# Optimization experiments

Measured on AMD Instinct MI355X. Metric: run time of the kernel, lower is better.

## Reference

```python
import jax, jax.numpy as jnp
import numpy as np

FEAT = 1024   # feat_dim
EMB = 64      # emb_dim
GROUP = 16    # group == fc_dim
DG = FEAT // GROUP  # 64, per-group query/key dim and conv out channels per group
R = 1024      # num_rois
N = 1024      # nongt_dim


def setup_inputs() -> dict:
    key = jax.random.key(0)
    ks = jax.random.split(key, 8)
    inp = {
        "position_embedding": jax.random.normal(ks[0], (R, N, EMB), dtype=jnp.float32),
        "roi_feat": jax.random.normal(ks[1], (R, FEAT), dtype=jnp.float32),
        # fc_q / fc_k: Linear(feat_dim, feat_dim)
        "Wq": jax.random.normal(ks[2], (FEAT, FEAT), dtype=jnp.float32) * 0.02,
        "bq": jnp.zeros((FEAT,), dtype=jnp.float32),
        "Wk": jax.random.normal(ks[3], (FEAT, FEAT), dtype=jnp.float32) * 0.02,
        "bk": jnp.zeros((FEAT,), dtype=jnp.float32),
        # fc_pos_feat: Linear(emb_dim, fc_dim=group)
        "Wp": jax.random.normal(ks[4], (GROUP, EMB), dtype=jnp.float32) * 0.1,
        "bp": jnp.zeros((GROUP,), dtype=jnp.float32),
        # conv_cat: Conv2d(group*feat_dim, feat_dim, k=1, groups=group)
        # per group g: in FEAT channels -> out DG channels. Shape [GROUP, DG, FEAT].
        "Wc": jax.random.normal(ks[5], (GROUP, DG, FEAT), dtype=jnp.float32) * 0.02,
        "bc": jnp.zeros((FEAT,), dtype=jnp.float32),
        "nongt_dim": N,
    }
    return inp


def reference(position_embedding, roi_feat, Wq, bq, Wk, bk, Wp, bp, Wc, bc, nongt_dim):
    scale = 1.0 / np.sqrt(float(DG))
    # fc_pos_feat + relu -> aff_weight [R, GROUP, N]
    pos_feat = jax.nn.relu(jnp.einsum("rne,ge->rng", position_embedding, Wp) + bp)
    aff_weight = jnp.transpose(pos_feat, (0, 2, 1))  # [R, GROUP, N]
    nongt = roi_feat[:nongt_dim]                     # [N, FEAT]
    q = (roi_feat @ Wq.T + bq).reshape(-1, GROUP, DG)   # [R, GROUP, DG]
    k = (nongt @ Wk.T + bk).reshape(-1, GROUP, DG)      # [N, GROUP, DG]
    # per-group QK^T with log position bias
    aff = jnp.einsum("rgd,ngd->rgn", q, k) * scale      # [R, GROUP, N]
    weighted = jnp.log(jnp.clip(aff_weight, 1e-6, None)) + aff
    att = jax.nn.softmax(weighted, axis=2)              # [R, GROUP, N]
    # attention * V -> [R, GROUP, FEAT]
    out_t = jnp.einsum("rgn,nf->rgf", att, nongt)
    # grouped 1x1 conv combine: group g maps FEAT -> DG output channels
    out = jnp.einsum("rgf,gof->rgo", out_t, Wc).reshape(-1, FEAT) + bc
    return out
```

## Files before the change

kernel.cpp:

```cpp
#include <hip/hip_runtime.h>

#define R_DIM 1024
#define N_DIM 1024
#define FEAT  1024
#define EMB   64
#define GROUP 16
#define DG    64

typedef _Float16 half8  __attribute__((ext_vector_type(8)));
typedef _Float16 half4v __attribute__((ext_vector_type(4)));
typedef float    f32x4  __attribute__((ext_vector_type(4)));

__global__ __launch_bounds__(256) void qk_gemm(
    const float* __restrict__ roi, const float* __restrict__ Wq,
    const float* __restrict__ bq,  const float* __restrict__ Wk,
    const float* __restrict__ bk,  _Float16* __restrict__ qh,
    _Float16* __restrict__ kh)
{
  __shared__ float aT[16][68];
  __shared__ float bqT[16][68];
  __shared__ float bkT[16][68];
  const int t  = threadIdx.x;
  const int r0 = blockIdx.x * 64, c0 = blockIdx.y * 64;
  const int lr = t >> 2, lk = (t & 3) << 2;
  const int ty = t >> 4, tx = t & 15;
  const float* ap  = roi + (r0 + lr) * FEAT + lk;
  const float* bqp = Wq  + (c0 + lr) * FEAT + lk;
  const float* bkp = Wk  + (c0 + lr) * FEAT + lk;
  float4 av  = *(const float4*)ap;
  float4 bqv = *(const float4*)bqp;
  float4 bkv = *(const float4*)bkp;
  float accq[4][4] = {}, acck[4][4] = {};
  for (int k0 = 0; k0 < FEAT; k0 += 16) {
    aT[lk+0][lr]=av.x;   aT[lk+1][lr]=av.y;   aT[lk+2][lr]=av.z;   aT[lk+3][lr]=av.w;
    bqT[lk+0][lr]=bqv.x; bqT[lk+1][lr]=bqv.y; bqT[lk+2][lr]=bqv.z; bqT[lk+3][lr]=bqv.w;
    bkT[lk+0][lr]=bkv.x; bkT[lk+1][lr]=bkv.y; bkT[lk+2][lr]=bkv.z; bkT[lk+3][lr]=bkv.w;
    __syncthreads();
    const bool more = (k0 + 16) < FEAT;
    float4 av_n, bqv_n, bkv_n;
    if (more) {
      av_n  = *(const float4*)(ap  + k0 + 16);
      bqv_n = *(const float4*)(bqp + k0 + 16);
      bkv_n = *(const float4*)(bkp + k0 + 16);
    }
#pragma unroll
    for (int kk = 0; kk < 16; ++kk) {
      const float4 a4 = *(const float4*)&aT[kk][ty << 2];
      const float4 q4 = *(const float4*)&bqT[kk][tx << 2];
      const float4 k4 = *(const float4*)&bkT[kk][tx << 2];
      const float ar[4] = {a4.x, a4.y, a4.z, a4.w};
      const float qr[4] = {q4.x, q4.y, q4.z, q4.w};
      const float kr[4] = {k4.x, k4.y, k4.z, k4.w};
#pragma unroll
      for (int i = 0; i < 4; ++i)
#pragma unroll
        for (int j = 0; j < 4; ++j) {
          accq[i][j] += ar[i] * qr[j];
          acck[i][j] += ar[i] * kr[j];
        }
    }
    __syncthreads();
    if (more) { av = av_n; bqv = bqv_n; bkv = bkv_n; }
  }
  const float4 bq4 = *(const float4*)(bq + c0 + (tx << 2));
  const float4 bk4 = *(const float4*)(bk + c0 + (tx << 2));
  const float bqr[4] = {bq4.x, bq4.y, bq4.z, bq4.w};
  const float bkr[4] = {bk4.x, bk4.y, bk4.z, bk4.w};
#pragma unroll
  for (int i = 0; i < 4; ++i) {
    half4v oq, ok;
#pragma unroll
    for (int j = 0; j < 4; ++j) {
      oq[j] = (_Float16)(accq[i][j] + bqr[j]);
      ok[j] = (_Float16)(acck[i][j] + bkr[j]);
    }
    const int row = r0 + (ty << 2) + i;
    *(half4v*)(qh + (size_t)row * FEAT + c0 + (tx << 2)) = oq;
    *(half4v*)(kh + (size_t)row * FEAT + c0 + (tx << 2)) = ok;
  }
}

__global__ __launch_bounds__(128) void pos_log(
    const float* __restrict__ pe, const float* __restrict__ Wp,
    const float* __restrict__ bp, _Float16* __restrict__ logw)
{
  __shared__ float tile[128 * 68];
  const int t    = threadIdx.x;
  const int base = blockIdx.x << 7;
  const int r    = base >> 10;
  const int n0   = base & 1023;
  const float* src = pe + ((size_t)base << 6);
#pragma unroll
  for (int i = 0; i < 16; ++i) {
    const int flat = (i << 7) + t;
    const int rl = flat >> 4, e4 = flat & 15;
    const float4 v = *(const float4*)(src + ((size_t)flat << 2));
    *(float4*)&tile[rl * 68 + (e4 << 2)] = v;
  }
  __syncthreads();
  float acc[16];
#pragma unroll
  for (int g = 0; g < 16; ++g) acc[g] = bp[g];
#pragma unroll
  for (int e4 = 0; e4 < 16; ++e4) {
    const float4 x = *(const float4*)&tile[t * 68 + (e4 << 2)];
#pragma unroll
    for (int g = 0; g < 16; ++g) {
      const float4 w = *(const float4*)(Wp + (g << 6) + (e4 << 2));
      acc[g] += x.x*w.x + x.y*w.y + x.z*w.z + x.w*w.w;
    }
  }
  const int n = n0 + t;
#pragma unroll
  for (int g = 0; g < 16; ++g) {
    const float v = fmaxf(acc[g], 1e-6f);
    logw[((size_t)((r << 4) + g) << 10) + n] = (_Float16)__logf(v);
  }
}

__global__ __launch_bounds__(256) void kc_gemm(
    const float* __restrict__ roi, const float* __restrict__ Wc,
    _Float16* __restrict__ kct)
{
  __shared__ float aT[16][68];
  __shared__ float bT[16][68];
  const int t  = threadIdx.x;
  const int n0 = blockIdx.x * 64;
  const int g  = blockIdx.y;
  const int lr = t >> 2, lk = (t & 3) << 2;
  const int ty = t >> 4, tx = t & 15;
  const float* ap  = Wc  + (size_t)(g * DG + lr) * FEAT + lk;
  const float* bp_ = roi + (size_t)(n0 + lr) * FEAT + lk;
  float4 av = *(const float4*)ap;
  float4 bv = *(const float4*)bp_;
  float acc[4][4] = {};
  for (int k0 = 0; k0 < FEAT; k0 += 16) {
    aT[lk+0][lr]=av.x; aT[lk+1][lr]=av.y; aT[lk+2][lr]=av.z; aT[lk+3][lr]=av.w;
    bT[lk+0][lr]=bv.x; bT[lk+1][lr]=bv.y; bT[lk+2][lr]=bv.z; bT[lk+3][lr]=bv.w;
    __syncthreads();
    const bool more = (k0 + 16) < FEAT;
    float4 av_n, bv_n;
    if (more) {
      av_n = *(const float4*)(ap  + k0 + 16);
      bv_n = *(const float4*)(bp_ + k0 + 16);
    }
#pragma unroll
    for (int kk = 0; kk < 16; ++kk) {
      const float4 a4 = *(const float4*)&aT[kk][ty << 2];
      const float4 b4 = *(const float4*)&bT[kk][tx << 2];
      const float ar[4] = {a4.x, a4.y, a4.z, a4.w};
      const float br[4] = {b4.x, b4.y, b4.z, b4.w};
#pragma unroll
      for (int i = 0; i < 4; ++i)
#pragma unroll
        for (int j = 0; j < 4; ++j) acc[i][j] += ar[i] * br[j];
    }
    __syncthreads();
    if (more) { av = av_n; bv = bv_n; }
  }
#pragma unroll
  for (int i = 0; i < 4; ++i) {
    half4v o4;
#pragma unroll
    for (int j = 0; j < 4; ++j) o4[j] = (_Float16)acc[i][j];
    *(half4v*)(kct + (size_t)((g << 6) + (ty << 2) + i) * N_DIM + n0 + (tx << 2)) = o4;
  }
}

#define PLD 1032
__global__ __launch_bounds__(256) void attn_mfma(
    const _Float16* __restrict__ qh, const _Float16* __restrict__ kh,
    const _Float16* __restrict__ logw, const _Float16* __restrict__ kct,
    const float* __restrict__ bc, float* __restrict__ outp)
{
  __shared__ __align__(16) _Float16 P[16][PLD];
  __shared__ float Ored[4][16][68];
  __shared__ float redm[4][16];
  __shared__ float redl[4][16];

  const int t   = threadIdx.x;
  const int w   = t >> 6;
  const int l   = t & 63;
  const int q16 = l & 15;
  const int q4  = l >> 4;
  const int g   = blockIdx.y;
  const int r0  = blockIdx.x << 4;
  const int nbase = w << 8;

  const half8* qp = (const half8*)(qh + (size_t)(r0 + q16) * FEAT + (g << 6) + (q4 << 3));
  const half8 a0 = qp[0];
  const half8 a1 = qp[4];

  f32x4 S[16];
#pragma unroll
  for (int i = 0; i < 16; ++i) S[i] = (f32x4){0.f, 0.f, 0.f, 0.f};
#pragma unroll
  for (int t16 = 0; t16 < 16; ++t16) {
    const int n0 = nbase + (t16 << 4);
    const half8* kp = (const half8*)(kh + (size_t)(n0 + q16) * FEAT + (g << 6) + (q4 << 3));
    S[t16] = __builtin_amdgcn_mfma_f32_16x16x32_f16(a0, kp[0], S[t16], 0, 0, 0);
    S[t16] = __builtin_amdgcn_mfma_f32_16x16x32_f16(a1, kp[4], S[t16], 0, 0, 0);
  }

#pragma unroll
  for (int t16 = 0; t16 < 16; ++t16) {
    const int n = nbase + (t16 << 4) + q16;
#pragma unroll
    for (int j = 0; j < 4; ++j) {
      const int r = r0 + (q4 << 2) + j;
      const float lw = (float)logw[(size_t)(((r << 4) + g) << 10) + n];
      S[t16][j] = S[t16][j] * 0.125f + lw;
    }
  }

  float m[4] = {-1e30f, -1e30f, -1e30f, -1e30f};
#pragma unroll
  for (int t16 = 0; t16 < 16; ++t16)
#pragma unroll
    for (int j = 0; j < 4; ++j) m[j] = fmaxf(m[j], S[t16][j]);
#pragma unroll
  for (int off = 8; off; off >>= 1)
#pragma unroll
    for (int j = 0; j < 4; ++j) m[j] = fmaxf(m[j], __shfl_xor(m[j], off));
  if (q16 == 0) {
#pragma unroll
    for (int j = 0; j < 4; ++j) redm[w][(q4 << 2) + j] = m[j];
  }
  __syncthreads();
#pragma unroll
  for (int j = 0; j < 4; ++j) {
    const int r = (q4 << 2) + j;
    m[j] = fmaxf(fmaxf(redm[0][r], redm[1][r]), fmaxf(redm[2][r], redm[3][r]));
  }

  float ls[4] = {0.f, 0.f, 0.f, 0.f};
#pragma unroll
  for (int t16 = 0; t16 < 16; ++t16) {
    const int n = nbase + (t16 << 4) + q16;
#pragma unroll
    for (int j = 0; j < 4; ++j) {
      const float p = __expf(S[t16][j] - m[j]);
      ls[j] += p;
      P[(q4 << 2) + j][n] = (_Float16)p;
    }
  }
#pragma unroll
  for (int off = 8; off; off >>= 1)
#pragma unroll
    for (int j = 0; j < 4; ++j) ls[j] += __shfl_xor(ls[j], off);
  if (q16 == 0) {
#pragma unroll
    for (int j = 0; j < 4; ++j) redl[w][(q4 << 2) + j] = ls[j];
  }
  __syncthreads();

  f32x4 O[4];
#pragma unroll
  for (int ot = 0; ot < 4; ++ot) O[ot] = (f32x4){0.f, 0.f, 0.f, 0.f};
#pragma unroll
  for (int ks = 0; ks < 8; ++ks) {
    const int nk = nbase + (ks << 5) + (q4 << 3);
    const half8 pa = *(const half8*)&P[q16][nk];
#pragma unroll
    for (int ot = 0; ot < 4; ++ot) {
      const half8 bfr = *(const half8*)(kct + (size_t)((g << 6) + (ot << 4) + q16) * N_DIM + nk);
      O[ot] = __builtin_amdgcn_mfma_f32_16x16x32_f16(pa, bfr, O[ot], 0, 0, 0);
    }
  }
#pragma unroll
  for (int ot = 0; ot < 4; ++ot)
#pragma unroll
    for (int j = 0; j < 4; ++j)
      Ored[w][(q4 << 2) + j][(ot << 4) + q16] = O[ot][j];
  __syncthreads();

  const int r  = t >> 4;
  const int o0 = (t & 15) << 2;
  const float lsum = redl[0][r] + redl[1][r] + redl[2][r] + redl[3][r];
  const float inv  = 1.0f / lsum;
  float o[4];
#pragma unroll
  for (int c = 0; c < 4; ++c)
    o[c] = Ored[0][r][o0 + c] + Ored[1][r][o0 + c] + Ored[2][r][o0 + c] + Ored[3][r][o0 + c];
  const float4 bcv = *(const float4*)(bc + (g << 6) + o0);
  float4 res;
  res.x = o[0] * inv + bcv.x;
  res.y = o[1] * inv + bcv.y;
  res.z = o[2] * inv + bcv.z;
  res.w = o[3] * inv + bcv.w;
  *(float4*)(outp + (size_t)(r0 + r) * FEAT + (g << 6) + o0) = res;
}

extern "C" void kernel_launch(void* const* d_in, const int* in_sizes, int n_in,
                              void* d_out, int out_size, void* d_ws, size_t ws_size,
                              hipStream_t stream)
{
  const float* pe  = (const float*)d_in[0];
  const float* roi = (const float*)d_in[1];
  const float* Wq  = (const float*)d_in[2];
  const float* bq  = (const float*)d_in[3];
  const float* Wk  = (const float*)d_in[4];
  const float* bk  = (const float*)d_in[5];
  const float* Wp  = (const float*)d_in[6];
  const float* bp  = (const float*)d_in[7];
  const float* Wc  = (const float*)d_in[8];
  const float* bc  = (const float*)d_in[9];
  float* outp = (float*)d_out;

  char* ws = (char*)d_ws;
  _Float16* qh   = (_Float16*)(ws);
  _Float16* kh   = (_Float16*)(ws + ((size_t)2 << 20));
  _Float16* kct  = (_Float16*)(ws + ((size_t)4 << 20));
  _Float16* logw = (_Float16*)(ws + ((size_t)6 << 20));

  qk_gemm<<<dim3(16, 16), 256, 0, stream>>>(roi, Wq, bq, Wk, bk, qh, kh);
  pos_log<<<8192, 128, 0, stream>>>(pe, Wp, bp, logw);
  kc_gemm<<<dim3(16, 16), 256, 0, stream>>>(roi, Wc, kct);
  attn_mfma<<<dim3(64, 16), 256, 0, stream>>>(qh, kh, logw, kct, bc, outp);
}
```

Measured before the change: 229.1 us.

## Merge producer kernels into one launch with MFMA GEMMs and restructured pos_log

Replaces the three producer kernels (Q/K projection, position-log, Wc·roi GEMM) with a single kernel whose block index picks the role. The GEMM roles now use fp16 MFMA 16x16x32 instructions, converting fp32 operands straight from global memory with no LDS staging. The position-log role keeps the transposed Wp in LDS and splits the embedding dimension across 4 lanes, reducing with shuffles. This cuts launch count and moves the projections onto matrix cores, at the cost of fp16 rounding of the GEMM inputs and uncoalesced strided loads and scalar fp16 stores.

```diff
diff --git a/kernel.cpp b/kernel.cpp
--- a/kernel.cpp
+++ b/kernel.cpp
@@ -11,159 +11,120 @@
 typedef _Float16 half4v __attribute__((ext_vector_type(4)));
 typedef float    f32x4  __attribute__((ext_vector_type(4)));
 
-__global__ __launch_bounds__(256) void qk_gemm(
+__device__ __forceinline__ half8 cvt8(const float* p) {
+  const float4 a = *(const float4*)p;
+  const float4 b = *(const float4*)(p + 4);
+  half8 h;
+  h[0] = (_Float16)a.x; h[1] = (_Float16)a.y; h[2] = (_Float16)a.z; h[3] = (_Float16)a.w;
+  h[4] = (_Float16)b.x; h[5] = (_Float16)b.y; h[6] = (_Float16)b.z; h[7] = (_Float16)b.w;
+  return h;
+}
+
+__global__ __launch_bounds__(256) void producers(
     const float* __restrict__ roi, const float* __restrict__ Wq,
     const float* __restrict__ bq,  const float* __restrict__ Wk,
-    const float* __restrict__ bk,  _Float16* __restrict__ qh,
-    _Float16* __restrict__ kh)
+    const float* __restrict__ bk,  const float* __restrict__ Wc,
+    const float* __restrict__ pe,  const float* __restrict__ Wp,
+    const float* __restrict__ bp,
+    _Float16* __restrict__ qh, _Float16* __restrict__ kh,
+    _Float16* __restrict__ kct, _Float16* __restrict__ logw)
 {
-  __shared__ float aT[16][68];
-  __shared__ float bqT[16][68];
-  __shared__ float bkT[16][68];
+  __shared__ float lds_w[4 * 264];
+  const int bx = blockIdx.x;
   const int t  = threadIdx.x;
-  const int r0 = blockIdx.x * 64, c0 = blockIdx.y * 64;
-  const int lr = t >> 2, lk = (t & 3) << 2;
-  const int ty = t >> 4, tx = t & 15;
-  const float* ap  = roi + (r0 + lr) * FEAT + lk;
-  const float* bqp = Wq  + (c0 + lr) * FEAT + lk;
-  const float* bkp = Wk  + (c0 + lr) * FEAT + lk;
-  float4 av  = *(const float4*)ap;
-  float4 bqv = *(const float4*)bqp;
-  float4 bkv = *(const float4*)bkp;
-  float accq[4][4] = {}, acck[4][4] = {};
-  for (int k0 = 0; k0 < FEAT; k0 += 16) {
-    aT[lk+0][lr]=av.x;   aT[lk+1][lr]=av.y;   aT[lk+2][lr]=av.z;   aT[lk+3][lr]=av.w;
-    bqT[lk+0][lr]=bqv.x; bqT[lk+1][lr]=bqv.y; bqT[lk+2][lr]=bqv.z; bqT[lk+3][lr]=bqv.w;
-    bkT[lk+0][lr]=bkv.x; bkT[lk+1][lr]=bkv.y; bkT[lk+2][lr]=bkv.z; bkT[lk+3][lr]=bkv.w;
+
+  if (bx < 768) {
+    const float* A; const float* B; const float* bias;
+    _Float16* outb; int r0, c0;
+    if (bx < 256) {
+      A = roi; B = Wq; bias = bq; outb = qh;
+      r0 = (bx >> 4) << 6; c0 = (bx & 15) << 6;
+    } else if (bx < 512) {
+      const int i = bx - 256;
+      A = roi; B = Wk; bias = bk; outb = kh;
+      r0 = (i >> 4) << 6; c0 = (i & 15) << 6;
+    } else {
+      const int i = bx - 512, g = i >> 4;
+      A = Wc + ((size_t)g << 16); B = roi; bias = nullptr;
+      outb = kct + ((size_t)g << 16);
+      r0 = 0; c0 = (i & 15) << 6;
+    }
+    const int wv = t >> 6, l = t & 63, q16 = l & 15, q4 = l >> 4;
+    const float* ap  = A + (size_t)(r0 + (wv << 4) + q16) * FEAT + (q4 << 3);
+    const float* bp0 = B + (size_t)(c0 + q16) * FEAT + (q4 << 3);
+
+    f32x4 acc[4];
+#pragma unroll
+    for (int ct = 0; ct < 4; ++ct) acc[ct] = (f32x4){0.f, 0.f, 0.f, 0.f};
+
+    for (int kk = 0; kk < FEAT; kk += 32) {
+      const half8 a = cvt8(ap + kk);
+#pragma unroll
+      for (int ct = 0; ct < 4; ++ct) {
+        const half8 b = cvt8(bp0 + (size_t)(ct << 4) * FEAT + kk);
+        acc[ct] = __builtin_amdgcn_mfma_f32_16x16x32_f16(a, b, acc[ct], 0, 0, 0);
+      }
+    }
+#pragma unroll
+    for (int ct = 0; ct < 4; ++ct) {
+      const int col = c0 + (ct << 4) + q16;
+      const float bv = bias ? bias[col] : 0.f;
+#pragma unroll
+      for (int j = 0; j < 4; ++j) {
+        const int row = r0 + (wv << 4) + (q4 << 2) + j;
+        outb[(size_t)row * FEAT + col] = (_Float16)(acc[ct][j] + bv);
+      }
+    }
+  } else {
+    {
+      const float4 v = ((const float4*)Wp)[t];
+      const int l4s = (t & 15) >> 2, ib = (t & 3) << 2, g = t >> 4;
+#pragma unroll
+      for (int c = 0; c < 4; ++c)
+        lds_w[l4s * 264 + (ib + c) * 16 + g] = ((const float*)&v)[c];
+    }
     __syncthreads();
-    const bool more = (k0 + 16) < FEAT;
-    float4 av_n, bqv_n, bkv_n;
-    if (more) {
-      av_n  = *(const float4*)(ap  + k0 + 16);
-      bqv_n = *(const float4*)(bqp + k0 + 16);
-      bkv_n = *(const float4*)(bkp + k0 + 16);
-    }
-#pragma unroll
-    for (int kk = 0; kk < 16; ++kk) {
-      const float4 a4 = *(const float4*)&aT[kk][ty << 2];
-      const float4 q4 = *(const float4*)&bqT[kk][tx << 2];
-      const float4 k4 = *(const float4*)&bkT[kk][tx << 2];
-      const float ar[4] = {a4.x, a4.y, a4.z, a4.w};
-      const float qr[4] = {q4.x, q4.y, q4.z, q4.w};
-      const float kr[4] = {k4.x, k4.y, k4.z, k4.w};
-#pragma unroll
-      for (int i = 0; i < 4; ++i)
-#pragma unroll
-        for (int j = 0; j < 4; ++j) {
-          accq[i][j] += ar[i] * qr[j];
-          acck[i][j] += ar[i] * kr[j];
+    const int w = t >> 6, l = t & 63, r16 = l >> 2, l4 = l & 3;
+    const float4 bpv = *(const float4*)(bp + (l4 << 2));
+    const int pb = bx - 768;
+#pragma unroll 1
+    for (int it = 0; it < 8; ++it) {
+      const int rowb = ((pb << 5) + (w << 3) + it) << 4;
+      const int row  = rowb + r16;
+      const float* src = pe + ((size_t)row << 6) + (l4 << 4);
+      float x[16];
+      *(float4*)&x[0]  = *(const float4*)(src);
+      *(float4*)&x[4]  = *(const float4*)(src + 4);
+      *(float4*)&x[8]  = *(const float4*)(src + 8);
+      *(float4*)&x[12] = *(const float4*)(src + 12);
+      float acc[16];
+#pragma unroll
+      for (int g = 0; g < 16; ++g) acc[g] = 0.f;
+#pragma unroll
+      for (int i = 0; i < 16; ++i) {
+#pragma unroll
+        for (int g4 = 0; g4 < 4; ++g4) {
+          const float4 w4 = *(const float4*)&lds_w[l4 * 264 + i * 16 + (g4 << 2)];
+          acc[(g4 << 2) + 0] += x[i] * w4.x;
+          acc[(g4 << 2) + 1] += x[i] * w4.y;
+          acc[(g4 << 2) + 2] += x[i] * w4.z;
+          acc[(g4 << 2) + 3] += x[i] * w4.w;
         }
-    }
-    __syncthreads();
-    if (more) { av = av_n; bqv = bqv_n; bkv = bkv_n; }
-  }
-  const float4 bq4 = *(const float4*)(bq + c0 + (tx << 2));
-  const float4 bk4 = *(const float4*)(bk + c0 + (tx << 2));
-  const float bqr[4] = {bq4.x, bq4.y, bq4.z, bq4.w};
-  const float bkr[4] = {bk4.x, bk4.y, bk4.z, bk4.w};
-#pragma unroll
-  for (int i = 0; i < 4; ++i) {
-    half4v oq, ok;
-#pragma unroll
-    for (int j = 0; j < 4; ++j) {
-      oq[j] = (_Float16)(accq[i][j] + bqr[j]);
-      ok[j] = (_Float16)(acck[i][j] + bkr[j]);
-    }
-    const int row = r0 + (ty << 2) + i;
-    *(half4v*)(qh + (size_t)row * FEAT + c0 + (tx << 2)) = oq;
-    *(half4v*)(kh + (size_t)row * FEAT + c0 + (tx << 2)) = ok;
-  }
-}
-
-__global__ __launch_bounds__(128) void pos_log(
-    const float* __restrict__ pe, const float* __restrict__ Wp,
-    const float* __restrict__ bp, _Float16* __restrict__ logw)
-{
-  __shared__ float tile[128 * 68];
-  const int t    = threadIdx.x;
-  const int base = blockIdx.x << 7;
-  const int r    = base >> 10;
-  const int n0   = base & 1023;
-  const float* src = pe + ((size_t)base << 6);
-#pragma unroll
-  for (int i = 0; i < 16; ++i) {
-    const int flat = (i << 7) + t;
-    const int rl = flat >> 4, e4 = flat & 15;
-    const float4 v = *(const float4*)(src + ((size_t)flat << 2));
-    *(float4*)&tile[rl * 68 + (e4 << 2)] = v;
-  }
-  __syncthreads();
-  float acc[16];
-#pragma unroll
-  for (int g = 0; g < 16; ++g) acc[g] = bp[g];
-#pragma unroll
-  for (int e4 = 0; e4 < 16; ++e4) {
-    const float4 x = *(const float4*)&tile[t * 68 + (e4 << 2)];
-#pragma unroll
-    for (int g = 0; g < 16; ++g) {
-      const float4 w = *(const float4*)(Wp + (g << 6) + (e4 << 2));
-      acc[g] += x.x*w.x + x.y*w.y + x.z*w.z + x.w*w.w;
-    }
-  }
-  const int n = n0 + t;
-#pragma unroll
-  for (int g = 0; g < 16; ++g) {
-    const float v = fmaxf(acc[g], 1e-6f);
-    logw[((size_t)((r << 4) + g) << 10) + n] = (_Float16)__logf(v);
-  }
-}
-
-__global__ __launch_bounds__(256) void kc_gemm(
-    const float* __restrict__ roi, const float* __restrict__ Wc,
-    _Float16* __restrict__ kct)
-{
-  __shared__ float aT[16][68];
-  __shared__ float bT[16][68];
-  const int t  = threadIdx.x;
-  const int n0 = blockIdx.x * 64;
-  const int g  = blockIdx.y;
-  const int lr = t >> 2, lk = (t & 3) << 2;
-  const int ty = t >> 4, tx = t & 15;
-  const float* ap  = Wc  + (size_t)(g * DG + lr) * FEAT + lk;
-  const float* bp_ = roi + (size_t)(n0 + lr) * FEAT + lk;
-  float4 av = *(const float4*)ap;
-  float4 bv = *(const float4*)bp_;
-  float acc[4][4] = {};
-  for (int k0 = 0; k0 < FEAT; k0 += 16) {
-    aT[lk+0][lr]=av.x; aT[lk+1][lr]=av.y; aT[lk+2][lr]=av.z; aT[lk+3][lr]=av.w;
-    bT[lk+0][lr]=bv.x; bT[lk+1][lr]=bv.y; bT[lk+2][lr]=bv.z; bT[lk+3][lr]=bv.w;
-    __syncthreads();
-    const bool more = (k0 + 16) < FEAT;
-    float4 av_n, bv_n;
-    if (more) {
-      av_n = *(const float4*)(ap  + k0 + 16);
-      bv_n = *(const float4*)(bp_ + k0 + 16);
-    }
-#pragma unroll
-    for (int kk = 0; kk < 16; ++kk) {
-      const float4 a4 = *(const float4*)&aT[kk][ty << 2];
-      const float4 b4 = *(const float4*)&bT[kk][tx << 2];
-      const float ar[4] = {a4.x, a4.y, a4.z, a4.w};
-      const float br[4] = {b4.x, b4.y, b4.z, b4.w};
-#pragma unroll
-      for (int i = 0; i < 4; ++i)
-#pragma unroll
-        for (int j = 0; j < 4; ++j) acc[i][j] += ar[i] * br[j];
-    }
-    __syncthreads();
-    if (more) { av = av_n; bv = bv_n; }
-  }
-#pragma unroll
-  for (int i = 0; i < 4; ++i) {
-    half4v o4;
-#pragma unroll
-    for (int j = 0; j < 4; ++j) o4[j] = (_Float16)acc[i][j];
-    *(half4v*)(kct + (size_t)((g << 6) + (ty << 2) + i) * N_DIM + n0 + (tx << 2)) = o4;
+      }
+#pragma unroll
+      for (int g = 0; g < 16; ++g) {
+        acc[g] += __shfl_xor(acc[g], 1);
+        acc[g] += __shfl_xor(acc[g], 2);
+      }
+      const int r = row >> 10, n = row & 1023;
+      _Float16* dst = logw + ((size_t)(r << 4) << 10) + n;
+#pragma unroll
+      for (int c = 0; c < 4; ++c) {
+        const int g = (l4 << 2) + c;
+        const float v = fmaxf(acc[g] + ((const float*)&bpv)[c], 1e-6f);
+        dst[(size_t)g << 10] = (_Float16)__logf(v);
+      }
+    }
   }
 }
 
@@ -313,8 +274,7 @@
   _Float16* kct  = (_Float16*)(ws + ((size_t)4 << 20));
   _Float16* logw = (_Float16*)(ws + ((size_t)6 << 20));
 
-  qk_gemm<<<dim3(16, 16), 256, 0, stream>>>(roi, Wq, bq, Wk, bk, qh, kh);
-  pos_log<<<8192, 128, 0, stream>>>(pe, Wp, bp, logw);
-  kc_gemm<<<dim3(16, 16), 256, 0, stream>>>(roi, Wc, kct);
+  producers<<<2816, 256, 0, stream>>>(roi, Wq, bq, Wk, bk, Wc, pe, Wp, bp,
+                                      qh, kh, kct, logw);
   attn_mfma<<<dim3(64, 16), 256, 0, stream>>>(qh, kh, logw, kct, bc, outp);
 }
```

Measured after the change: 292.7 us. 27.7% more time.

## Compute position-embedding projection with fp16 MFMA and coalesced transposed stores

Applied to the files above, without the earlier changes.

Replaces the scalar FP32 pos_log kernel with pos_mfma. It converts each 128x64 position-embedding tile to fp16 in an XOR-swizzled LDS buffer and computes the 16-group projection with 16x16x32 f16 MFMA instructions. The log outputs are staged in LDS and written as coalesced half8 rows, replacing the earlier scattered 2-byte stores. The aim is to make this 256MB-read stage bandwidth-bound rather than ALU-bound. The cost is reduced precision in the projection inputs, which are now rounded to fp16.

```diff
diff --git a/kernel.cpp b/kernel.cpp
--- a/kernel.cpp
+++ b/kernel.cpp
@@ -10,6 +10,15 @@
 typedef _Float16 half8  __attribute__((ext_vector_type(8)));
 typedef _Float16 half4v __attribute__((ext_vector_type(4)));
 typedef float    f32x4  __attribute__((ext_vector_type(4)));
+
+__device__ __forceinline__ half8 cvt8(const float* p) {
+  const float4 a = *(const float4*)p;
+  const float4 b = *(const float4*)(p + 4);
+  half8 h;
+  h[0] = (_Float16)a.x; h[1] = (_Float16)a.y; h[2] = (_Float16)a.z; h[3] = (_Float16)a.w;
+  h[4] = (_Float16)b.x; h[5] = (_Float16)b.y; h[6] = (_Float16)b.z; h[7] = (_Float16)b.w;
+  return h;
+}
 
 __global__ __launch_bounds__(256) void qk_gemm(
     const float* __restrict__ roi, const float* __restrict__ Wq,
@@ -80,42 +89,61 @@
   }
 }
 
-__global__ __launch_bounds__(128) void pos_log(
+__global__ __launch_bounds__(256) void pos_mfma(
     const float* __restrict__ pe, const float* __restrict__ Wp,
     const float* __restrict__ bp, _Float16* __restrict__ logw)
 {
-  __shared__ float tile[128 * 68];
-  const int t    = threadIdx.x;
-  const int base = blockIdx.x << 7;
-  const int r    = base >> 10;
-  const int n0   = base & 1023;
-  const float* src = pe + ((size_t)base << 6);
-#pragma unroll
-  for (int i = 0; i < 16; ++i) {
-    const int flat = (i << 7) + t;
-    const int rl = flat >> 4, e4 = flat & 15;
-    const float4 v = *(const float4*)(src + ((size_t)flat << 2));
-    *(float4*)&tile[rl * 68 + (e4 << 2)] = v;
-  }
-  __syncthreads();
-  float acc[16];
-#pragma unroll
-  for (int g = 0; g < 16; ++g) acc[g] = bp[g];
-#pragma unroll
-  for (int e4 = 0; e4 < 16; ++e4) {
-    const float4 x = *(const float4*)&tile[t * 68 + (e4 << 2)];
-#pragma unroll
-    for (int g = 0; g < 16; ++g) {
-      const float4 w = *(const float4*)(Wp + (g << 6) + (e4 << 2));
-      acc[g] += x.x*w.x + x.y*w.y + x.z*w.z + x.w*w.w;
-    }
-  }
-  const int n = n0 + t;
-#pragma unroll
-  for (int g = 0; g < 16; ++g) {
-    const float v = fmaxf(acc[g], 1e-6f);
-    logw[((size_t)((r << 4) + g) << 10) + n] = (_Float16)__logf(v);
-  }
+  __shared__ __align__(16) _Float16 Xs[128 * 64];
+  __shared__ __align__(16) _Float16 LW[16][136];
+  const int t  = threadIdx.x;
+  const int bx = blockIdx.x;
+  const int r  = bx >> 3;
+  const int n0 = (bx & 7) << 7;
+  const size_t gbase = ((size_t)bx << 13);
+
+#pragma unroll
+  for (int i = 0; i < 8; ++i) {
+    const int flat4 = (i << 8) + t;
+    const int row = flat4 >> 4, e4 = flat4 & 15;
+    const float4 v = *(const float4*)(pe + gbase + ((size_t)flat4 << 2));
+    half4v h;
+    h[0] = (_Float16)v.x; h[1] = (_Float16)v.y;
+    h[2] = (_Float16)v.z; h[3] = (_Float16)v.w;
+    const int boff = (row << 7) + (((e4 << 3)) ^ ((row & 7) << 4));
+    *(half4v*)((char*)Xs + boff) = h;
+  }
+
+  const int w = t >> 6, l = t & 63, q16 = l & 15, q4 = l >> 4;
+  const float* wpp = Wp + (q16 << 6) + (q4 << 3);
+  const half8 wb0 = cvt8(wpp);
+  const half8 wb1 = cvt8(wpp + 32);
+  const float bpg = bp[q16];
+  __syncthreads();
+
+#pragma unroll
+  for (int tt = 0; tt < 2; ++tt) {
+    const int lrbase = (w << 5) + (tt << 4);
+    const int lr = lrbase + q16;
+    const int b0 = (lr << 7) + (((q4 << 4))      ^ ((lr & 7) << 4));
+    const int b1 = (lr << 7) + (((q4 << 4) + 64) ^ ((lr & 7) << 4));
+    const half8 a0 = *(const half8*)((const char*)Xs + b0);
+    const half8 a1 = *(const half8*)((const char*)Xs + b1);
+    f32x4 acc = (f32x4){0.f, 0.f, 0.f, 0.f};
+    acc = __builtin_amdgcn_mfma_f32_16x16x32_f16(a0, wb0, acc, 0, 0, 0);
+    acc = __builtin_amdgcn_mfma_f32_16x16x32_f16(a1, wb1, acc, 0, 0, 0);
+    half4v o;
+#pragma unroll
+    for (int j = 0; j < 4; ++j) {
+      const float v = fmaxf(acc[j] + bpg, 1e-6f);
+      o[j] = (_Float16)__logf(v);
+    }
+    *(half4v*)&LW[q16][lrbase + (q4 << 2)] = o;
+  }
+  __syncthreads();
+
+  const int g = t >> 4, n4 = t & 15;
+  const half8 vv = *(const half8*)&LW[g][n4 << 3];
+  *(half8*)(logw + ((size_t)((r << 4) + g) << 10) + n0 + (n4 << 3)) = vv;
 }
 
 __global__ __launch_bounds__(256) void kc_gemm(
@@ -314,7 +342,7 @@
   _Float16* logw = (_Float16*)(ws + ((size_t)6 << 20));
 
   qk_gemm<<<dim3(16, 16), 256, 0, stream>>>(roi, Wq, bq, Wk, bk, qh, kh);
-  pos_log<<<8192, 128, 0, stream>>>(pe, Wp, bp, logw);
+  pos_mfma<<<8192, 256, 0, stream>>>(pe, Wp, bp, logw);
   kc_gemm<<<dim3(16, 16), 256, 0, stream>>>(roi, Wc, kct);
   attn_mfma<<<dim3(64, 16), 256, 0, stream>>>(qh, kh, logw, kct, bc, outp);
 }
```

New measurement: 201.8 us. 11.9% less time.
